# Kernel tuning notes

Hardware: AMD Instinct MI355X
Metric: run time of the kernel (lower is better)

## Reference

```python
import jax, jax.numpy as jnp
import numpy as np

LOG2PI = float(np.log(2.0 * np.pi))
MIN_DURATION = 1
NUM_STATES = 512
OBS_DIM = 128
B, T, K = 64, 2000, 400


def setup_inputs() -> dict:
    key = jax.random.key(0)
    ks = jax.random.split(key, 10)
    observations = jax.random.normal(ks[0], (B, T, OBS_DIM), dtype=jnp.float32)
    state_sequence = jax.random.randint(ks[1], (B, K), 0, NUM_STATES, dtype=jnp.int32)
    # durations >= min_duration so gamma log-prob stays finite
    duration_sequence = jax.random.randint(ks[2], (B, K), 1, 51, dtype=jnp.int32)
    # learned parameters, initialized as in the torch module
    alpha_params = jnp.ones((NUM_STATES,), jnp.float32)
    beta_params = jnp.ones((NUM_STATES,), jnp.float32)
    transition_logits = jax.random.normal(ks[3], (NUM_STATES, NUM_STATES), dtype=jnp.float32)
    initial_logits = jnp.zeros((NUM_STATES,), jnp.float32)
    observation_means = jax.random.normal(ks[4], (NUM_STATES, OBS_DIM), dtype=jnp.float32)
    observation_logvars = jnp.zeros((NUM_STATES, OBS_DIM), jnp.float32)
    return {
        "observations": observations,
        "alpha_params": alpha_params,
        "beta_params": beta_params,
        "transition_logits": transition_logits,
        "initial_logits": initial_logits,
        "observation_means": observation_means,
        "observation_logvars": observation_logvars,
        "state_sequence": state_sequence,
        "duration_sequence": duration_sequence,
    }


def _gamma_duration_logprob(alpha_params, beta_params, state_sequence, duration_sequence):
    # fully vectorized version of the per-sample Python loop in DurationModel
    d = duration_sequence.astype(jnp.float32)                      # [B, K]
    alpha = jax.nn.softplus(alpha_params)[state_sequence] + 1e-6   # [B, K]
    beta = jax.nn.softplus(beta_params)[state_sequence] + 1e-6
    lp = (alpha - 1.0) * jnp.log(d + 1e-8) - beta * d
    lp = lp - (jax.lax.lgamma(alpha) - alpha * jnp.log(beta))
    return jnp.where(d >= MIN_DURATION, lp, -jnp.inf)


def reference(observations, alpha_params, beta_params, transition_logits,
              initial_logits, observation_means, observation_logvars,
              state_sequence, duration_sequence):
    # --- duration log-probs per segment: [B, K]
    log_dur = _gamma_duration_logprob(alpha_params, beta_params,
                                      state_sequence, duration_sequence)

    # --- expand segments to frames: frame t belongs to segment with cum[idx-1] <= t < cum[idx]
    cum = jnp.cumsum(duration_sequence, axis=1)                    # [B, K]
    t = jnp.arange(observations.shape[1])                          # [T]
    seg_idx = jax.vmap(lambda c: jnp.searchsorted(c, t, side='right'))(cum)
    seg_idx = jnp.clip(seg_idx, 0, state_sequence.shape[1] - 1)    # [B, T]
    frame_states = jnp.take_along_axis(state_sequence, seg_idx, axis=1)  # [B, T]

    # --- diagonal-gaussian observation log-probs per frame: [B, T]
    mu = observation_means[frame_states]                           # [B, T, D]
    lv = observation_logvars[frame_states]                         # [B, T, D]
    resid2 = (observations - mu) ** 2 * jnp.exp(-lv)
    log_obs = -0.5 * jnp.sum(lv + resid2 + LOG2PI, axis=-1)        # [B, T]

    # --- initial + transition log-probs over the segment-level state chain
    log_trans = jax.nn.log_softmax(transition_logits, axis=-1)     # [S, S]
    log_init = jax.nn.log_softmax(initial_logits)                  # [S]
    trans_lp = log_trans[state_sequence[:, :-1], state_sequence[:, 1:]].sum(axis=1)  # [B]
    init_lp = log_init[state_sequence[:, 0]]                       # [B]

    # --- per-sequence supervised log-likelihood: [B]
    log_likelihood = log_obs.sum(axis=1) + log_dur.sum(axis=1) + trans_lp + init_lp
    return log_likelihood
```

## Files before the change

kernel.cpp:

```cpp
#include <hip/hip_runtime.h>
#include <hip/hip_bf16.h>
#include <math.h>

#define NS 512
#define OD 128
#define BB 64
#define TT 2000
#define KK 400
#define CHUNK 128
#define NCH 16
#define LOG2PI_F 1.8378770664093453f
#define SEQ_OFF  576
#define PART_OFF 1024


__device__ __forceinline__ float softplusf(float x) {
    return (x > 20.f) ? x : log1pf(expf(x));
}

__global__ __launch_bounds__(256) void big_kernel(
    const float* __restrict__ obs, const float* __restrict__ mu,
    const float* __restrict__ lvar, const float* __restrict__ trans,
    const float* __restrict__ init_logits,
    const float* __restrict__ alpha_p, const float* __restrict__ beta_p,
    const int* __restrict__ states, const int* __restrict__ durs,
    float* __restrict__ ws)
{
    const int tid = threadIdx.x;
    const int bid = blockIdx.x;
    __shared__ float red[4];

    if (bid < BB * NCH) {
        const int b = bid >> 4;
        const int t0 = (bid & 15) * CHUNK;

        __shared__ int fsl[CHUNK];
        __shared__ int csum[8];

        const int lane = tid & 63, w = tid >> 6;
        int s0v = states[b * KK + tid];
        int d0  = durs[b * KK + tid];
        int s1v = 0, d1 = 0;
        if (tid + 256 < KK) {
            s1v = states[b * KK + tid + 256];
            d1  = durs[b * KK + tid + 256];
        }
        int v0 = d0, v1 = d1;
        #pragma unroll
        for (int off = 1; off < 64; off <<= 1) {
            int u0 = __shfl_up(v0, off, 64);
            int u1 = __shfl_up(v1, off, 64);
            if (lane >= off) { v0 += u0; v1 += u1; }
        }
        if (lane == 63) { csum[w] = v0; csum[4 + w] = v1; }
        __syncthreads();
        int off0 = 0, off1 = 0;
        #pragma unroll
        for (int c = 0; c < 8; ++c) {
            int cs = csum[c];
            off0 += (c < w) ? cs : 0;
            off1 += (c < 4 + w) ? cs : 0;
        }
        const int c0 = v0 + off0;
        const int c1 = v1 + off1;

        {
            int a = c0 - d0, e = c0;
            a = (a < t0) ? t0 : a;
            e = (e > t0 + CHUNK) ? t0 + CHUNK : e;
            for (int t = a; t < e; ++t) fsl[t - t0] = s0v;
            int a1 = c1 - d1, e1 = (tid + 256 == KK - 1) ? t0 + CHUNK : c1;
            a1 = (a1 < t0) ? t0 : a1;
            e1 = (e1 > t0 + CHUNK) ? t0 + CHUNK : e1;
            for (int t = a1; t < e1; ++t) fsl[t - t0] = s1v;
        }
        __syncthreads();

        const int row = tid >> 5;
        const int dd = (tid & 31) * 4;
        const float* obase = obs + ((size_t)b * TT + t0) * OD + dd;
        float acc = 0.f;
        if (t0 + CHUNK <= TT) {
            #pragma unroll
            for (int g = 0; g < 2; ++g) {
                float4 ov[8];
                #pragma unroll
                for (int j = 0; j < 8; ++j)
                    ov[j] = *(const float4*)(obase
                              + (size_t)((g * 8 + j) * 8 + row) * OD);
                #pragma unroll
                for (int j = 0; j < 8; ++j) {
                    const int s = fsl[(g * 8 + j) * 8 + row];
                    const float4 m  = *(const float4*)(mu  + (size_t)s * OD + dd);
                    const float4 lv = *(const float4*)(lvar + (size_t)s * OD + dd);
                    const float dx = ov[j].x - m.x, dy = ov[j].y - m.y,
                                dz = ov[j].z - m.z, dw = ov[j].w - m.w;
                    acc += lv.x + lv.y + lv.z + lv.w + 4.f * LOG2PI_F
                         + dx * dx * __expf(-lv.x) + dy * dy * __expf(-lv.y)
                         + dz * dz * __expf(-lv.z) + dw * dw * __expf(-lv.w);
                }
            }
        } else {
            #pragma unroll
            for (int i = 0; i < CHUNK / 8; ++i) {
                const int t = t0 + i * 8 + row;
                if (t < TT) {
                    const int s = fsl[i * 8 + row];
                    const float4 o  = *(const float4*)(obs + ((size_t)(b * TT + t)) * OD + dd);
                    const float4 m  = *(const float4*)(mu  + (size_t)s * OD + dd);
                    const float4 lv = *(const float4*)(lvar + (size_t)s * OD + dd);
                    const float dx = o.x - m.x, dy = o.y - m.y, dz = o.z - m.z, dw = o.w - m.w;
                    acc += lv.x + lv.y + lv.z + lv.w + 4.f * LOG2PI_F
                         + dx * dx * __expf(-lv.x) + dy * dy * __expf(-lv.y)
                         + dz * dz * __expf(-lv.z) + dw * dw * __expf(-lv.w);
                }
            }
        }
        for (int off = 32; off; off >>= 1) acc += __shfl_down(acc, off, 64);
        if ((tid & 63) == 0) red[tid >> 6] = acc;
        __syncthreads();
        if (tid == 0)
            ws[PART_OFF + bid] = -0.5f * (red[0] + red[1] + red[2] + red[3]);
    } else if (bid < BB * NCH + NS + 1) {
        const int r = bid - BB * NCH;
        const float* src = (r < NS) ? (trans + (size_t)r * NS) : init_logits;
        float x0 = src[tid];
        float x1 = src[tid + 256];
        float m = fmaxf(x0, x1);
        for (int off = 32; off; off >>= 1) m = fmaxf(m, __shfl_down(m, off, 64));
        if ((tid & 63) == 0) red[tid >> 6] = m;
        __syncthreads();
        m = fmaxf(fmaxf(red[0], red[1]), fmaxf(red[2], red[3]));
        __syncthreads();
        float e = __expf(x0 - m) + __expf(x1 - m);
        for (int off = 32; off; off >>= 1) e += __shfl_down(e, off, 64);
        if ((tid & 63) == 0) red[tid >> 6] = e;
        __syncthreads();
        if (tid == 0)
            ws[(r < NS) ? r : 512] = m + __logf(red[0] + red[1] + red[2] + red[3]);
    } else {
        const int b = bid - (BB * NCH + NS + 1);
        float lp = 0.f;
        for (int k = tid; k < KK; k += 256) {
            const int s = states[b * KK + k];
            const float dv = (float)durs[b * KK + k];
            const float a  = softplusf(alpha_p[s]) + 1e-6f;
            const float bt = softplusf(beta_p[s]) + 1e-6f;
            float v = (a - 1.f) * __logf(dv + 1e-8f) - bt * dv
                    + a * __logf(bt) - lgammaf(a);
            lp += (dv >= 1.f) ? v : -INFINITY;
            if (k < KK - 1)
                lp += trans[(size_t)s * NS + states[b * KK + k + 1]];
        }
        for (int off = 32; off; off >>= 1) lp += __shfl_down(lp, off, 64);
        if ((tid & 63) == 0) red[tid >> 6] = lp;
        __syncthreads();
        if (tid == 0)
            ws[SEQ_OFF + b] = red[0] + red[1] + red[2] + red[3]
                            + init_logits[states[b * KK]];
    }
}

__global__ __launch_bounds__(256) void fin_kernel(
    const int* __restrict__ states, const float* __restrict__ ws,
    float* __restrict__ out)
{
    const int b = blockIdx.x;
    const int tid = threadIdx.x;
    __shared__ float red[4];

    float lp = 0.f;
    if (tid < NCH)       lp = ws[PART_OFF + b * NCH + tid];
    else if (tid == NCH) lp = ws[SEQ_OFF + b] - ws[512];
    for (int k = tid; k < KK - 1; k += 256)
        lp -= ws[states[b * KK + k]];
    for (int off = 32; off; off >>= 1) lp += __shfl_down(lp, off, 64);
    if ((tid & 63) == 0) red[tid >> 6] = lp;
    __syncthreads();
    if (tid == 0)
        out[b] = red[0] + red[1] + red[2] + red[3];
}

extern "C" void kernel_launch(void* const* d_in, const int* in_sizes, int n_in,
                              void* d_out, int out_size, void* d_ws, size_t ws_size,
                              hipStream_t stream) {
    const float* observations = (const float*)d_in[0];
    const float* alpha_p      = (const float*)d_in[1];
    const float* beta_p       = (const float*)d_in[2];
    const float* trans        = (const float*)d_in[3];
    const float* init_logits  = (const float*)d_in[4];
    const float* obs_means    = (const float*)d_in[5];
    const float* obs_logvars  = (const float*)d_in[6];
    const int*   state_seq    = (const int*)d_in[7];
    const int*   dur_seq      = (const int*)d_in[8];

    float* ws = (float*)d_ws;
    float* out = (float*)d_out;

    big_kernel<<<BB * NCH + NS + 1 + BB, 256, 0, stream>>>(
        observations, obs_means, obs_logvars, trans, init_logits,
        alpha_p, beta_p, state_seq, dur_seq, ws);
    fin_kernel<<<BB, 256, 0, stream>>>(state_seq, ws, out);
}
```

Before: 23.79 us.

## Split logsumexp into a first kernel and fuse finalization via atomics

Moves the transition and initial logsumexp blocks into a separate first kernel that also zeroes the output. The main kernel now subtracts the row normalizers inline and accumulates per-sequence partials into the output with atomicAdd, which removes the final reduction kernel. It also replaces lgammaf with a Lanczos approximation and simplifies the observation loop by dropping the explicit 8-deep prefetch batch. The kernel count stays at two, but the atomics make the float summation order nondeterministic, and the simpler loop may lose some memory-level parallelism.

```diff
diff --git a/kernel.cpp b/kernel.cpp
--- a/kernel.cpp
+++ b/kernel.cpp
@@ -10,21 +10,59 @@
 #define CHUNK 128
 #define NCH 16
 #define LOG2PI_F 1.8378770664093453f
-#define SEQ_OFF  576
-#define PART_OFF 1024
 
 
 __device__ __forceinline__ float softplusf(float x) {
     return (x > 20.f) ? x : log1pf(expf(x));
 }
 
-__global__ __launch_bounds__(256) void big_kernel(
+__device__ __forceinline__ float gammlnf(float x) {
+    float tmp = x + 5.5f;
+    tmp -= (x + 0.5f) * __logf(tmp);
+    const float ser = 1.000000000190015f
+        + 76.18009172947146f    / (x + 1.f)
+        - 86.50532032941677f    / (x + 2.f)
+        + 24.01409824083091f    / (x + 3.f)
+        - 1.231739572450155f    / (x + 4.f)
+        + 1.208650973866179e-3f / (x + 5.f)
+        - 5.395239384953e-6f    / (x + 6.f);
+    return -tmp + __logf(2.5066282746310005f * ser / x);
+}
+
+__global__ __launch_bounds__(256) void k1_kernel(
+    const float* __restrict__ trans, const float* __restrict__ init_logits,
+    float* __restrict__ ws, float* __restrict__ out)
+{
+    const int tid = threadIdx.x;
+    const int bid = blockIdx.x;
+    __shared__ float red[4];
+
+    if (bid == NS && tid < BB) out[tid] = 0.f;
+
+    const float* src = (bid < NS) ? (trans + (size_t)bid * NS) : init_logits;
+    float x0 = src[tid];
+    float x1 = src[tid + 256];
+    float m = fmaxf(x0, x1);
+    for (int off = 32; off; off >>= 1) m = fmaxf(m, __shfl_down(m, off, 64));
+    if ((tid & 63) == 0) red[tid >> 6] = m;
+    __syncthreads();
+    m = fmaxf(fmaxf(red[0], red[1]), fmaxf(red[2], red[3]));
+    __syncthreads();
+    float e = __expf(x0 - m) + __expf(x1 - m);
+    for (int off = 32; off; off >>= 1) e += __shfl_down(e, off, 64);
+    if ((tid & 63) == 0) red[tid >> 6] = e;
+    __syncthreads();
+    if (tid == 0)
+        ws[(bid < NS) ? bid : 512] = m + __logf(red[0] + red[1] + red[2] + red[3]);
+}
+
+__global__ __launch_bounds__(256) void k2_kernel(
     const float* __restrict__ obs, const float* __restrict__ mu,
     const float* __restrict__ lvar, const float* __restrict__ trans,
     const float* __restrict__ init_logits,
     const float* __restrict__ alpha_p, const float* __restrict__ beta_p,
     const int* __restrict__ states, const int* __restrict__ durs,
-    float* __restrict__ ws)
+    const float* __restrict__ ws, float* __restrict__ out)
 {
     const int tid = threadIdx.x;
     const int bid = blockIdx.x;
@@ -78,27 +116,19 @@
 
         const int row = tid >> 5;
         const int dd = (tid & 31) * 4;
-        const float* obase = obs + ((size_t)b * TT + t0) * OD + dd;
         float acc = 0.f;
         if (t0 + CHUNK <= TT) {
             #pragma unroll
-            for (int g = 0; g < 2; ++g) {
-                float4 ov[8];
-                #pragma unroll
-                for (int j = 0; j < 8; ++j)
-                    ov[j] = *(const float4*)(obase
-                              + (size_t)((g * 8 + j) * 8 + row) * OD);
-                #pragma unroll
-                for (int j = 0; j < 8; ++j) {
-                    const int s = fsl[(g * 8 + j) * 8 + row];
-                    const float4 m  = *(const float4*)(mu  + (size_t)s * OD + dd);
-                    const float4 lv = *(const float4*)(lvar + (size_t)s * OD + dd);
-                    const float dx = ov[j].x - m.x, dy = ov[j].y - m.y,
-                                dz = ov[j].z - m.z, dw = ov[j].w - m.w;
-                    acc += lv.x + lv.y + lv.z + lv.w + 4.f * LOG2PI_F
-                         + dx * dx * __expf(-lv.x) + dy * dy * __expf(-lv.y)
-                         + dz * dz * __expf(-lv.z) + dw * dw * __expf(-lv.w);
-                }
+            for (int i = 0; i < CHUNK / 8; ++i) {
+                const int t = t0 + i * 8 + row;
+                const int s = fsl[i * 8 + row];
+                const float4 o  = *(const float4*)(obs + ((size_t)(b * TT + t)) * OD + dd);
+                const float4 m  = *(const float4*)(mu  + (size_t)s * OD + dd);
+                const float4 lv = *(const float4*)(lvar + (size_t)s * OD + dd);
+                const float dx = o.x - m.x, dy = o.y - m.y, dz = o.z - m.z, dw = o.w - m.w;
+                acc += lv.x + lv.y + lv.z + lv.w + 4.f * LOG2PI_F
+                     + dx * dx * __expf(-lv.x) + dy * dy * __expf(-lv.y)
+                     + dz * dz * __expf(-lv.z) + dw * dw * __expf(-lv.w);
             }
         } else {
             #pragma unroll
@@ -120,26 +150,9 @@
         if ((tid & 63) == 0) red[tid >> 6] = acc;
         __syncthreads();
         if (tid == 0)
-            ws[PART_OFF + bid] = -0.5f * (red[0] + red[1] + red[2] + red[3]);
-    } else if (bid < BB * NCH + NS + 1) {
-        const int r = bid - BB * NCH;
-        const float* src = (r < NS) ? (trans + (size_t)r * NS) : init_logits;
-        float x0 = src[tid];
-        float x1 = src[tid + 256];
-        float m = fmaxf(x0, x1);
-        for (int off = 32; off; off >>= 1) m = fmaxf(m, __shfl_down(m, off, 64));
-        if ((tid & 63) == 0) red[tid >> 6] = m;
-        __syncthreads();
-        m = fmaxf(fmaxf(red[0], red[1]), fmaxf(red[2], red[3]));
-        __syncthreads();
-        float e = __expf(x0 - m) + __expf(x1 - m);
-        for (int off = 32; off; off >>= 1) e += __shfl_down(e, off, 64);
-        if ((tid & 63) == 0) red[tid >> 6] = e;
-        __syncthreads();
-        if (tid == 0)
-            ws[(r < NS) ? r : 512] = m + __logf(red[0] + red[1] + red[2] + red[3]);
+            atomicAdd(out + b, -0.5f * (red[0] + red[1] + red[2] + red[3]));
     } else {
-        const int b = bid - (BB * NCH + NS + 1);
+        const int b = bid - BB * NCH;
         float lp = 0.f;
         for (int k = tid; k < KK; k += 256) {
             const int s = states[b * KK + k];
@@ -147,38 +160,19 @@
             const float a  = softplusf(alpha_p[s]) + 1e-6f;
             const float bt = softplusf(beta_p[s]) + 1e-6f;
             float v = (a - 1.f) * __logf(dv + 1e-8f) - bt * dv
-                    + a * __logf(bt) - lgammaf(a);
+                    + a * __logf(bt) - gammlnf(a);
             lp += (dv >= 1.f) ? v : -INFINITY;
             if (k < KK - 1)
-                lp += trans[(size_t)s * NS + states[b * KK + k + 1]];
+                lp += trans[(size_t)s * NS + states[b * KK + k + 1]] - ws[s];
         }
+        if (tid == 0)
+            lp += init_logits[states[b * KK]] - ws[512];
         for (int off = 32; off; off >>= 1) lp += __shfl_down(lp, off, 64);
         if ((tid & 63) == 0) red[tid >> 6] = lp;
         __syncthreads();
         if (tid == 0)
-            ws[SEQ_OFF + b] = red[0] + red[1] + red[2] + red[3]
-                            + init_logits[states[b * KK]];
+            atomicAdd(out + b, red[0] + red[1] + red[2] + red[3]);
     }
-}
-
-__global__ __launch_bounds__(256) void fin_kernel(
-    const int* __restrict__ states, const float* __restrict__ ws,
-    float* __restrict__ out)
-{
-    const int b = blockIdx.x;
-    const int tid = threadIdx.x;
-    __shared__ float red[4];
-
-    float lp = 0.f;
-    if (tid < NCH)       lp = ws[PART_OFF + b * NCH + tid];
-    else if (tid == NCH) lp = ws[SEQ_OFF + b] - ws[512];
-    for (int k = tid; k < KK - 1; k += 256)
-        lp -= ws[states[b * KK + k]];
-    for (int off = 32; off; off >>= 1) lp += __shfl_down(lp, off, 64);
-    if ((tid & 63) == 0) red[tid >> 6] = lp;
-    __syncthreads();
-    if (tid == 0)
-        out[b] = red[0] + red[1] + red[2] + red[3];
 }
 
 extern "C" void kernel_launch(void* const* d_in, const int* in_sizes, int n_in,
@@ -197,8 +191,8 @@
     float* ws = (float*)d_ws;
     float* out = (float*)d_out;
 
-    big_kernel<<<BB * NCH + NS + 1 + BB, 256, 0, stream>>>(
+    k1_kernel<<<NS + 1, 256, 0, stream>>>(trans, init_logits, ws, out);
+    k2_kernel<<<BB * NCH + BB, 256, 0, stream>>>(
         observations, obs_means, obs_logvars, trans, init_logits,
-        alpha_p, beta_p, state_seq, dur_seq, ws);
-    fin_kernel<<<BB, 256, 0, stream>>>(state_seq, ws, out);
+        alpha_p, beta_p, state_seq, dur_seq, ws, out);
 }
```

New measurement: 27.32 us. +14.9%, slower.

## Double block size to 512 threads and replace lgammaf with Lanczos approximation

Applied to the files above, without the earlier changes.

Launches the fused kernel with 512 threads per block so each thread handles one segment or softmax element and fewer time rows, and drops the batched register-prefetch of observation rows in favour of a simple strided loop. The per-sequence duration path replaces the library lgammaf with an inline Lanczos approximation built on fast logs. The aim is more in-flight threads per block and a cheaper log-gamma, at the cost of less per-thread load batching and a small change in numerical accuracy.

```diff
diff --git a/kernel.cpp b/kernel.cpp
--- a/kernel.cpp
+++ b/kernel.cpp
@@ -18,7 +18,20 @@
     return (x > 20.f) ? x : log1pf(expf(x));
 }
 
-__global__ __launch_bounds__(256) void big_kernel(
+__device__ __forceinline__ float gammlnf(float x) {
+    float tmp = x + 5.5f;
+    tmp -= (x + 0.5f) * __logf(tmp);
+    const float ser = 1.000000000190015f
+        + 76.18009172947146f    / (x + 1.f)
+        - 86.50532032941677f    / (x + 2.f)
+        + 24.01409824083091f    / (x + 3.f)
+        - 1.231739572450155f    / (x + 4.f)
+        + 1.208650973866179e-3f / (x + 5.f)
+        - 5.395239384953e-6f    / (x + 6.f);
+    return -tmp + __logf(2.5066282746310005f * ser / x);
+}
+
+__global__ __launch_bounds__(512, 8) void big_kernel(
     const float* __restrict__ obs, const float* __restrict__ mu,
     const float* __restrict__ lvar, const float* __restrict__ trans,
     const float* __restrict__ init_logits,
@@ -28,7 +41,7 @@
 {
     const int tid = threadIdx.x;
     const int bid = blockIdx.x;
-    __shared__ float red[4];
+    __shared__ float red[8];
 
     if (bid < BB * NCH) {
         const int b = bid >> 4;
@@ -38,74 +51,52 @@
         __shared__ int csum[8];
 
         const int lane = tid & 63, w = tid >> 6;
-        int s0v = states[b * KK + tid];
-        int d0  = durs[b * KK + tid];
-        int s1v = 0, d1 = 0;
-        if (tid + 256 < KK) {
-            s1v = states[b * KK + tid + 256];
-            d1  = durs[b * KK + tid + 256];
-        }
-        int v0 = d0, v1 = d1;
+        int sv = 0, dv = 0;
+        if (tid < KK) { sv = states[b * KK + tid]; dv = durs[b * KK + tid]; }
+        int v = dv;
         #pragma unroll
         for (int off = 1; off < 64; off <<= 1) {
-            int u0 = __shfl_up(v0, off, 64);
-            int u1 = __shfl_up(v1, off, 64);
-            if (lane >= off) { v0 += u0; v1 += u1; }
-        }
-        if (lane == 63) { csum[w] = v0; csum[4 + w] = v1; }
-        __syncthreads();
-        int off0 = 0, off1 = 0;
+            int u = __shfl_up(v, off, 64);
+            if (lane >= off) v += u;
+        }
+        if (lane == 63) csum[w] = v;
+        __syncthreads();
+        int woff = 0;
         #pragma unroll
-        for (int c = 0; c < 8; ++c) {
-            int cs = csum[c];
-            off0 += (c < w) ? cs : 0;
-            off1 += (c < 4 + w) ? cs : 0;
-        }
-        const int c0 = v0 + off0;
-        const int c1 = v1 + off1;
-
-        {
-            int a = c0 - d0, e = c0;
+        for (int c = 0; c < 8; ++c) woff += (c < w) ? csum[c] : 0;
+        const int cum = v + woff;
+
+        if (tid < KK) {
+            int a = cum - dv;
+            int e = (tid == KK - 1) ? t0 + CHUNK : cum;
             a = (a < t0) ? t0 : a;
             e = (e > t0 + CHUNK) ? t0 + CHUNK : e;
-            for (int t = a; t < e; ++t) fsl[t - t0] = s0v;
-            int a1 = c1 - d1, e1 = (tid + 256 == KK - 1) ? t0 + CHUNK : c1;
-            a1 = (a1 < t0) ? t0 : a1;
-            e1 = (e1 > t0 + CHUNK) ? t0 + CHUNK : e1;
-            for (int t = a1; t < e1; ++t) fsl[t - t0] = s1v;
+            for (int t = a; t < e; ++t) fsl[t - t0] = sv;
         }
         __syncthreads();
 
         const int row = tid >> 5;
         const int dd = (tid & 31) * 4;
-        const float* obase = obs + ((size_t)b * TT + t0) * OD + dd;
         float acc = 0.f;
         if (t0 + CHUNK <= TT) {
             #pragma unroll
-            for (int g = 0; g < 2; ++g) {
-                float4 ov[8];
-                #pragma unroll
-                for (int j = 0; j < 8; ++j)
-                    ov[j] = *(const float4*)(obase
-                              + (size_t)((g * 8 + j) * 8 + row) * OD);
-                #pragma unroll
-                for (int j = 0; j < 8; ++j) {
-                    const int s = fsl[(g * 8 + j) * 8 + row];
-                    const float4 m  = *(const float4*)(mu  + (size_t)s * OD + dd);
-                    const float4 lv = *(const float4*)(lvar + (size_t)s * OD + dd);
-                    const float dx = ov[j].x - m.x, dy = ov[j].y - m.y,
-                                dz = ov[j].z - m.z, dw = ov[j].w - m.w;
-                    acc += lv.x + lv.y + lv.z + lv.w + 4.f * LOG2PI_F
-                         + dx * dx * __expf(-lv.x) + dy * dy * __expf(-lv.y)
-                         + dz * dz * __expf(-lv.z) + dw * dw * __expf(-lv.w);
-                }
+            for (int i = 0; i < CHUNK / 16; ++i) {
+                const int t = t0 + i * 16 + row;
+                const int s = fsl[i * 16 + row];
+                const float4 o  = *(const float4*)(obs + ((size_t)(b * TT + t)) * OD + dd);
+                const float4 m  = *(const float4*)(mu  + (size_t)s * OD + dd);
+                const float4 lv = *(const float4*)(lvar + (size_t)s * OD + dd);
+                const float dx = o.x - m.x, dy = o.y - m.y, dz = o.z - m.z, dw = o.w - m.w;
+                acc += lv.x + lv.y + lv.z + lv.w + 4.f * LOG2PI_F
+                     + dx * dx * __expf(-lv.x) + dy * dy * __expf(-lv.y)
+                     + dz * dz * __expf(-lv.z) + dw * dw * __expf(-lv.w);
             }
         } else {
             #pragma unroll
-            for (int i = 0; i < CHUNK / 8; ++i) {
-                const int t = t0 + i * 8 + row;
+            for (int i = 0; i < CHUNK / 16; ++i) {
+                const int t = t0 + i * 16 + row;
                 if (t < TT) {
-                    const int s = fsl[i * 8 + row];
+                    const int s = fsl[i * 16 + row];
                     const float4 o  = *(const float4*)(obs + ((size_t)(b * TT + t)) * OD + dd);
                     const float4 m  = *(const float4*)(mu  + (size_t)s * OD + dd);
                     const float4 lv = *(const float4*)(lvar + (size_t)s * OD + dd);
@@ -119,45 +110,57 @@
         for (int off = 32; off; off >>= 1) acc += __shfl_down(acc, off, 64);
         if ((tid & 63) == 0) red[tid >> 6] = acc;
         __syncthreads();
-        if (tid == 0)
-            ws[PART_OFF + bid] = -0.5f * (red[0] + red[1] + red[2] + red[3]);
+        if (tid == 0) {
+            float s = 0.f;
+            #pragma unroll
+            for (int c = 0; c < 8; ++c) s += red[c];
+            ws[PART_OFF + bid] = -0.5f * s;
+        }
     } else if (bid < BB * NCH + NS + 1) {
         const int r = bid - BB * NCH;
         const float* src = (r < NS) ? (trans + (size_t)r * NS) : init_logits;
-        float x0 = src[tid];
-        float x1 = src[tid + 256];
-        float m = fmaxf(x0, x1);
+        const float x = src[tid];
+        float m = x;
         for (int off = 32; off; off >>= 1) m = fmaxf(m, __shfl_down(m, off, 64));
         if ((tid & 63) == 0) red[tid >> 6] = m;
         __syncthreads();
-        m = fmaxf(fmaxf(red[0], red[1]), fmaxf(red[2], red[3]));
-        __syncthreads();
-        float e = __expf(x0 - m) + __expf(x1 - m);
+        m = red[0];
+        #pragma unroll
+        for (int c = 1; c < 8; ++c) m = fmaxf(m, red[c]);
+        __syncthreads();
+        float e = __expf(x - m);
         for (int off = 32; off; off >>= 1) e += __shfl_down(e, off, 64);
         if ((tid & 63) == 0) red[tid >> 6] = e;
         __syncthreads();
-        if (tid == 0)
-            ws[(r < NS) ? r : 512] = m + __logf(red[0] + red[1] + red[2] + red[3]);
+        if (tid == 0) {
+            float s = 0.f;
+            #pragma unroll
+            for (int c = 0; c < 8; ++c) s += red[c];
+            ws[(r < NS) ? r : 512] = m + __logf(s);
+        }
     } else {
         const int b = bid - (BB * NCH + NS + 1);
         float lp = 0.f;
-        for (int k = tid; k < KK; k += 256) {
-            const int s = states[b * KK + k];
-            const float dv = (float)durs[b * KK + k];
+        if (tid < KK) {
+            const int s = states[b * KK + tid];
+            const float dvf = (float)durs[b * KK + tid];
             const float a  = softplusf(alpha_p[s]) + 1e-6f;
             const float bt = softplusf(beta_p[s]) + 1e-6f;
-            float v = (a - 1.f) * __logf(dv + 1e-8f) - bt * dv
-                    + a * __logf(bt) - lgammaf(a);
-            lp += (dv >= 1.f) ? v : -INFINITY;
-            if (k < KK - 1)
-                lp += trans[(size_t)s * NS + states[b * KK + k + 1]];
+            float vv = (a - 1.f) * __logf(dvf + 1e-8f) - bt * dvf
+                     + a * __logf(bt) - gammlnf(a);
+            lp = (dvf >= 1.f) ? vv : -INFINITY;
+            if (tid < KK - 1)
+                lp += trans[(size_t)s * NS + states[b * KK + tid + 1]];
         }
         for (int off = 32; off; off >>= 1) lp += __shfl_down(lp, off, 64);
         if ((tid & 63) == 0) red[tid >> 6] = lp;
         __syncthreads();
-        if (tid == 0)
-            ws[SEQ_OFF + b] = red[0] + red[1] + red[2] + red[3]
-                            + init_logits[states[b * KK]];
+        if (tid == 0) {
+            float s = 0.f;
+            #pragma unroll
+            for (int c = 0; c < 8; ++c) s += red[c];
+            ws[SEQ_OFF + b] = s + init_logits[states[b * KK]];
+        }
     }
 }
 
@@ -197,7 +200,7 @@
     float* ws = (float*)d_ws;
     float* out = (float*)d_out;
 
-    big_kernel<<<BB * NCH + NS + 1 + BB, 256, 0, stream>>>(
+    big_kernel<<<BB * NCH + NS + 1 + BB, 512, 0, stream>>>(
         observations, obs_means, obs_logvars, trans, init_logits,
         alpha_p, beta_p, state_seq, dur_seq, ws);
     fin_kernel<<<BB, 256, 0, stream>>>(state_seq, ws, out);
```

Result: faster. 22.41 us (-5.8%).
